# Kernel tuning notes

Measured on AMD Instinct MI355X. Metric: run time of the kernel, lower is better.

## Reference

```python
import jax, jax.numpy as jnp
import numpy as np

N_NODES = 65536
N_EDGES = 1048576
IN_FEATS = 128
H1 = 128
H2 = 256
N_CLASSES = 16


def setup_inputs() -> dict:
    key = jax.random.key(0)
    ks = jax.random.split(key, 12)
    s = 0.05
    x = jax.random.normal(ks[0], (N_NODES, IN_FEATS), dtype=jnp.float32)
    src = jax.random.randint(ks[1], (N_EDGES,), 0, N_NODES, dtype=jnp.int32)
    dst = jax.random.randint(ks[2], (N_EDGES,), 0, N_NODES, dtype=jnp.int32)
    # SAGEConv('pool') params: fc_pool (bias), fc_self (no bias), fc_neigh (no bias), output bias
    Wp = jax.random.normal(ks[3], (H1, IN_FEATS), dtype=jnp.float32) * s
    bp = jnp.zeros((H1,), dtype=jnp.float32)
    Ws = jax.random.normal(ks[4], (H1, IN_FEATS), dtype=jnp.float32) * s
    Wn = jax.random.normal(ks[5], (H1, H1), dtype=jnp.float32) * s
    bn = jnp.zeros((H1,), dtype=jnp.float32)
    # MLP head
    W1 = jax.random.normal(ks[6], (H2, H1), dtype=jnp.float32) * s
    b1 = jnp.zeros((H2,), dtype=jnp.float32)
    W2 = jax.random.normal(ks[7], (N_CLASSES, H2), dtype=jnp.float32) * s
    b2 = jnp.zeros((N_CLASSES,), dtype=jnp.float32)
    return {"x": x, "Wp": Wp, "bp": bp, "Ws": Ws, "Wn": Wn, "bn": bn,
            "W1": W1, "b1": b1, "W2": W2, "b2": b2, "src": src, "dst": dst}


def reference(x, Wp, bp, Ws, Wn, bn, W1, b1, W2, b2, src, dst):
    N = x.shape[0]
    # SAGEConv 'pool': per-edge MLP on gathered source features, segment-max over dst
    m = jax.nn.relu(x[src] @ Wp.T + bp)              # [E, H1]
    pooled = jax.ops.segment_max(m, dst, num_segments=N)  # [N, H1], -inf for isolated
    pooled = jnp.where(jnp.isneginf(pooled), 0.0, pooled)
    h = x @ Ws.T + pooled @ Wn.T + bn                # combine self + neigh
    h = jax.nn.leaky_relu(h)                         # slope 0.01 matches torch default
    h = jax.nn.leaky_relu(h @ W1.T + b1)
    # dropout is identity in eval mode
    h = jax.nn.sigmoid(h @ W2.T + b2)
    return h
```

## Files before the change

### kernel.cpp

```cpp
#include <hip/hip_runtime.h>
#include <cstdint>
#include <cstddef>

typedef __attribute__((ext_vector_type(8))) __bf16 bf16x8;
typedef __attribute__((ext_vector_type(4))) float f32x4;

union bf8pack { unsigned short u[8]; bf16x8 v; uint4 q; };

#define BCAP 768

static __device__ __forceinline__ unsigned short f2b(float f) {
    union { float f; unsigned int u; } v; v.f = f;
    unsigned int u = v.u;
    unsigned int r = (u + 0x7fffu + ((u >> 16) & 1u)) >> 16;
    return (unsigned short)r;
}

__global__ __launch_bounds__(256) void scatter_conv(
    const int* __restrict__ src, const int* __restrict__ dst,
    int* __restrict__ bcnt, unsigned int* __restrict__ pairs,
    const float* __restrict__ Wp, const float* __restrict__ Ws,
    const float* __restrict__ Wn, const float* __restrict__ W1,
    const float* __restrict__ W2,
    unsigned short* __restrict__ Wp_b, unsigned short* __restrict__ Wcat,
    unsigned short* __restrict__ W1_b, unsigned short* __restrict__ W2_b)
{
    const int tid = threadIdx.x;
    if ((int)blockIdx.x >= 256) {
        int i = ((int)blockIdx.x - 256) * 256 + tid;
        if (i < 16384) {
            Wp_b[i] = f2b(Wp[i]);
        } else if (i < 49152) {
            int j = i - 16384; int o = j >> 8, k = j & 255;
            Wcat[j] = f2b(k < 128 ? Ws[o * 128 + k] : Wn[o * 128 + (k - 128)]);
        } else if (i < 81920) {
            W1_b[i - 49152] = f2b(W1[i - 49152]);
        } else if (i < 86016) {
            W2_b[i - 81920] = f2b(W2[i - 81920]);
        }
        return;
    }
    __shared__ int h[2048];
    __shared__ int base_l[2048];
    __shared__ int cnt[2048];
    for (int i = tid; i < 2048; i += 256) { h[i] = 0; cnt[i] = 0; }
    __syncthreads();
    int base = blockIdx.x * 4096;
    int d_r[16], s_r[16];
#pragma unroll
    for (int i = 0; i < 16; i++) {
        int e = base + i * 256 + tid;
        d_r[i] = dst[e]; s_r[i] = src[e];
        atomicAdd(&h[((unsigned)d_r[i]) >> 5], 1);
    }
    __syncthreads();
    for (int i = tid; i < 2048; i += 256)
        base_l[i] = h[i] ? (i * BCAP + atomicAdd(&bcnt[i], h[i])) : 0;
    __syncthreads();
#pragma unroll
    for (int i = 0; i < 16; i++) {
        int b = ((unsigned)d_r[i]) >> 5;
        int pos = base_l[b] + atomicAdd(&cnt[b], 1);
        if (pos < (b + 1) * BCAP)
            pairs[pos] = ((unsigned)s_r[i] << 5) | ((unsigned)d_r[i] & 31u);
    }
}

__global__ __launch_bounds__(256) void k1_fused(
    const float* __restrict__ x, const unsigned short* __restrict__ Wp_b,
    const float* __restrict__ bias, unsigned short* __restrict__ bufX,
    unsigned short* __restrict__ y)
{
    const int bm = blockIdx.x;
    const int w  = threadIdx.x >> 6;
    const int wm = w & 1, wn = w >> 1;
    const int l  = threadIdx.x & 63;
    const int lr = l & 15, quad = l >> 4;
    const int m0 = bm * 128 + wm * 64;
    const int n0 = wn * 64;

    f32x4 acc[4][4];
#pragma unroll
    for (int i = 0; i < 4; i++)
#pragma unroll
        for (int j = 0; j < 4; j++) acc[i][j] = (f32x4){0.f, 0.f, 0.f, 0.f};

    const float* Ap = x + (size_t)(m0 + lr) * 128 + quad * 8;
    const unsigned short* Bp = Wp_b + (size_t)(n0 + lr) * 128 + quad * 8;

#pragma unroll
    for (int ks = 0; ks < 4; ks++) {
        bf16x8 af[4], bf[4];
#pragma unroll
        for (int i = 0; i < 4; i++) {
            const float* p = Ap + (size_t)i * 16 * 128 + ks * 32;
            float4 f0 = *(const float4*)p;
            float4 f1 = *(const float4*)(p + 4);
            bf8pack pk;
            pk.u[0] = f2b(f0.x); pk.u[1] = f2b(f0.y);
            pk.u[2] = f2b(f0.z); pk.u[3] = f2b(f0.w);
            pk.u[4] = f2b(f1.x); pk.u[5] = f2b(f1.y);
            pk.u[6] = f2b(f1.z); pk.u[7] = f2b(f1.w);
            af[i] = pk.v;
            if (wn == 0)
                *(uint4*)(bufX + (size_t)(m0 + lr + i * 16) * 256 + ks * 32 + quad * 8) = pk.q;
        }
#pragma unroll
        for (int i = 0; i < 4; i++)
            bf[i] = *(const bf16x8*)(Bp + (size_t)i * 16 * 128 + ks * 32);
#pragma unroll
        for (int mi = 0; mi < 4; mi++)
#pragma unroll
            for (int ni = 0; ni < 4; ni++)
                acc[mi][ni] = __builtin_amdgcn_mfma_f32_16x16x32_bf16(
                    af[mi], bf[ni], acc[mi][ni], 0, 0, 0);
    }

#pragma unroll
    for (int ni = 0; ni < 4; ni++) {
        const int col = n0 + ni * 16 + lr;
        const float bv = bias[col];
#pragma unroll
        for (int mi = 0; mi < 4; mi++) {
#pragma unroll
            for (int r = 0; r < 4; r++) {
                const int row = m0 + mi * 16 + quad * 4 + r;
                float v = acc[mi][ni][r] + bv;
                v = v > 0.f ? v : 0.f;
                y[(size_t)row * 128 + col] = f2b(v);
            }
        }
    }
}

__global__ __launch_bounds__(256) void bucket_pool3(
    const unsigned int* __restrict__ yu, const int* __restrict__ bcnt,
    const unsigned int* __restrict__ pairs, unsigned short* __restrict__ bufX)
{
    __shared__ unsigned short ldsSrc[1024];
    __shared__ int bin[32], offl[32], cnt2[32];
    const int b = blockIdx.x;
    const int tid = threadIdx.x;
    if (tid < 32) { bin[tid] = 0; cnt2[tid] = 0; }
    __syncthreads();
    const int beg = b * BCAP;
    int nb = bcnt[b]; nb = nb < 1024 ? nb : 1024;

    for (int i = tid; i < nb; i += 256)
        atomicAdd(&bin[pairs[beg + i] & 31u], 1);
    __syncthreads();
    if (tid == 0) {
        int run = 0;
        for (int i = 0; i < 32; i++) { offl[i] = run; run += bin[i]; }
    }
    __syncthreads();
    for (int i = tid; i < nb; i += 256) {
        unsigned int p = pairs[beg + i];
        int d = p & 31u;
        int slot = offl[d] + atomicAdd(&cnt2[d], 1);
        ldsSrc[slot] = (unsigned short)(p >> 5);
    }
    __syncthreads();

    const int w = tid >> 6, lane = tid & 63;
    for (int ni = 0; ni < 8; ni++) {
        const int n = w * 8 + ni;
        const int e0 = offl[n], cnt = bin[n];
        float ax = 0.f, ay = 0.f;
        for (int e = 0; e < cnt; e += 8) {
            int s[8]; unsigned int v[8];
#pragma unroll
            for (int j = 0; j < 8; j++) {
                int idx = e + j; idx = idx < cnt ? idx : cnt - 1;
                s[j] = ldsSrc[e0 + idx];
            }
#pragma unroll
            for (int j = 0; j < 8; j++) v[j] = yu[(size_t)s[j] * 64 + lane];
#pragma unroll
            for (int j = 0; j < 8; j++) {
                ax = fmaxf(ax, __uint_as_float(v[j] << 16));
                ay = fmaxf(ay, __uint_as_float(v[j] & 0xffff0000u));
            }
        }
        unsigned int packed = (__float_as_uint(ax) >> 16) | (__float_as_uint(ay) & 0xffff0000u);
        ((unsigned int*)bufX)[(size_t)(b * 32 + n) * 128 + 64 + lane] = packed;
    }
}

__global__ __launch_bounds__(256) void k4_gemm(
    const unsigned short* __restrict__ A,
    const unsigned short* __restrict__ W,
    const float* __restrict__ bias,
    unsigned short* __restrict__ C)
{
    const int bm = (int)blockIdx.x;
    const int w  = threadIdx.x >> 6;
    const int wm = w & 1, wn = w >> 1;
    const int l  = threadIdx.x & 63;
    const int lr = l & 15, quad = l >> 4;
    const int m0 = bm * 128 + wm * 64;
    const int n0 = wn * 64;

    f32x4 acc[4][4];
#pragma unroll
    for (int i = 0; i < 4; i++)
#pragma unroll
        for (int j = 0; j < 4; j++) acc[i][j] = (f32x4){0.f, 0.f, 0.f, 0.f};

    const unsigned short* Ap = A + (size_t)(m0 + lr) * 256 + quad * 8;
    const unsigned short* Bp = W + (size_t)(n0 + lr) * 256 + quad * 8;

    for (int ks = 0; ks < 8; ks++) {
        bf16x8 af[4], bf[4];
#pragma unroll
        for (int i = 0; i < 4; i++)
            af[i] = *(const bf16x8*)(Ap + (size_t)i * 16 * 256 + ks * 32);
#pragma unroll
        for (int i = 0; i < 4; i++)
            bf[i] = *(const bf16x8*)(Bp + (size_t)i * 16 * 256 + ks * 32);
#pragma unroll
        for (int mi = 0; mi < 4; mi++)
#pragma unroll
            for (int ni = 0; ni < 4; ni++)
                acc[mi][ni] = __builtin_amdgcn_mfma_f32_16x16x32_bf16(
                    af[mi], bf[ni], acc[mi][ni], 0, 0, 0);
    }

#pragma unroll
    for (int ni = 0; ni < 4; ni++) {
        const int col = n0 + ni * 16 + lr;
        const float bv = bias[col];
#pragma unroll
        for (int mi = 0; mi < 4; mi++) {
#pragma unroll
            for (int r = 0; r < 4; r++) {
                const int row = m0 + mi * 16 + quad * 4 + r;
                float v = acc[mi][ni][r] + bv;
                v = v > 0.f ? v : 0.01f * v;
                C[(size_t)row * 128 + col] = f2b(v);
            }
        }
    }
}

__global__ __launch_bounds__(256) void k5_head(
    const unsigned short* __restrict__ hbuf, const unsigned short* __restrict__ W1_b,
    const float* __restrict__ b1, const unsigned short* __restrict__ W2_b,
    const float* __restrict__ b2, float* __restrict__ out)
{
    __shared__ unsigned short H2[64 * 264];
    const int tid = threadIdx.x;
    const int w = tid >> 6, l = tid & 63;
    const int lr = l & 15, quad = l >> 4;
    const int wm = w & 1, wn = w >> 1;
    const int row0 = blockIdx.x * 64;

    f32x4 acc[2][8];
#pragma unroll
    for (int i = 0; i < 2; i++)
#pragma unroll
        for (int j = 0; j < 8; j++) acc[i][j] = (f32x4){0.f, 0.f, 0.f, 0.f};

    const unsigned short* Ag = hbuf + (size_t)(row0 + wm * 32 + lr) * 128 + quad * 8;
    const unsigned short* Bp = W1_b + (size_t)(wn * 128 + lr) * 128 + quad * 8;

#pragma unroll
    for (int ks = 0; ks < 4; ks++) {
        bf16x8 af[2], bfr[8];
#pragma unroll
        for (int i = 0; i < 2; i++)
            af[i] = *(const bf16x8*)(Ag + (size_t)i * 16 * 128 + ks * 32);
#pragma unroll
        for (int i = 0; i < 8; i++)
            bfr[i] = *(const bf16x8*)(Bp + (size_t)i * 16 * 128 + ks * 32);
#pragma unroll
        for (int mi = 0; mi < 2; mi++)
#pragma unroll
            for (int ni = 0; ni < 8; ni++)
                acc[mi][ni] = __builtin_amdgcn_mfma_f32_16x16x32_bf16(
                    af[mi], bfr[ni], acc[mi][ni], 0, 0, 0);
    }

#pragma unroll
    for (int ni = 0; ni < 8; ni++) {
        const int col = wn * 128 + ni * 16 + lr;
        const float bv = b1[col];
#pragma unroll
        for (int mi = 0; mi < 2; mi++) {
#pragma unroll
            for (int r = 0; r < 4; r++) {
                const int row = wm * 32 + mi * 16 + quad * 4 + r;
                float v = acc[mi][ni][r] + bv;
                v = v > 0.f ? v : 0.01f * v;
                H2[row * 264 + col] = f2b(v);
            }
        }
    }
    __syncthreads();

    const int m0 = w * 16;
    f32x4 a2 = (f32x4){0.f, 0.f, 0.f, 0.f};
#pragma unroll
    for (int ks = 0; ks < 8; ks++) {
        bf16x8 a = *(const bf16x8*)&H2[(m0 + lr) * 264 + ks * 32 + quad * 8];
        bf16x8 bb = *(const bf16x8*)(W2_b + (size_t)lr * 256 + ks * 32 + quad * 8);
        a2 = __builtin_amdgcn_mfma_f32_16x16x32_bf16(a, bb, a2, 0, 0, 0);
    }
    const float bv = b2[lr];
#pragma unroll
    for (int r = 0; r < 4; r++) {
        const int row = row0 + m0 + quad * 4 + r;
        float v = a2[r] + bv;
        out[(size_t)row * 16 + lr] = 1.f / (1.f + __expf(-v));
    }
}

extern "C" void kernel_launch(void* const* d_in, const int* in_sizes, int n_in,
                              void* d_out, int out_size, void* d_ws, size_t ws_size,
                              hipStream_t stream)
{
    const float* x  = (const float*)d_in[0];
    const float* Wp = (const float*)d_in[1];
    const float* bp = (const float*)d_in[2];
    const float* Ws = (const float*)d_in[3];
    const float* Wn = (const float*)d_in[4];
    const float* bn = (const float*)d_in[5];
    const float* W1 = (const float*)d_in[6];
    const float* b1 = (const float*)d_in[7];
    const float* W2 = (const float*)d_in[8];
    const float* b2 = (const float*)d_in[9];
    const int* src  = (const int*)d_in[10];
    const int* dst  = (const int*)d_in[11];
    float* out = (float*)d_out;

    const int N = in_sizes[0] / 128;

    unsigned short* bufX = (unsigned short*)d_ws;
    unsigned short* y    = (unsigned short*)((char*)d_ws + (size_t)32 * 1024 * 1024);
    unsigned short* hbuf = (unsigned short*)((char*)d_ws + (size_t)48 * 1024 * 1024);

    unsigned short* Wp_b = (unsigned short*)((char*)d_ws + (size_t)96 * 1024 * 1024);
    unsigned short* Wcat = Wp_b + 16384;
    unsigned short* W1_b = Wcat + 32768;
    unsigned short* W2_b = W1_b + 32768;
    int* bcnt = (int*)(W2_b + 4096);
    unsigned int* pairs = (unsigned int*)(bcnt + 2048);

    dim3 blk(256);

    hipMemsetAsync(bcnt, 0, 2048 * sizeof(int), stream);

    scatter_conv<<<592, blk, 0, stream>>>(src, dst, bcnt, pairs,
                                          Wp, Ws, Wn, W1, W2,
                                          Wp_b, Wcat, W1_b, W2_b);

    k1_fused<<<N / 128, blk, 0, stream>>>(x, Wp_b, bp, bufX, y);

    bucket_pool3<<<2048, blk, 0, stream>>>((const unsigned int*)y, bcnt, pairs, bufX);

    k4_gemm<<<N / 128, blk, 0, stream>>>(bufX, Wcat, bn, hbuf);

    k5_head<<<N / 64, blk, 0, stream>>>(hbuf, W1_b, b1, W2_b, b2, out);
}
```

Before: 218.3 us.

## Merge scatter, weight conversion and edge GEMM; fuse combine GEMM into MLP head

The edge-binning scatter, the weight conversion and the x·Wp GEMM now run as one launch. The GEMM converts Wp from fp32 inline, so it no longer depends on a separate conversion pass. The self/neighbour combine GEMM is folded into the head kernel: it reads x directly (converting to bf16) plus a compact pooled buffer, and keeps the hidden activation in LDS. This removes the bf16 copy of x and the hbuf round trip, cuts two launches, and uses vectorised int4 index loads. In exchange, the head kernel needs more LDS and recomputes the x conversion, and the edge GEMM does redundant fp32→bf16 conversion of Wp in every block.

```diff
diff --git a/kernel.cpp b/kernel.cpp
--- a/kernel.cpp
+++ b/kernel.cpp
@@ -16,43 +16,117 @@
     return (unsigned short)r;
 }
 
-__global__ __launch_bounds__(256) void scatter_conv(
+static __device__ __forceinline__ bf16x8 cvt8(const float* __restrict__ p) {
+    float4 f0 = *(const float4*)p;
+    float4 f1 = *(const float4*)(p + 4);
+    bf8pack pk;
+    pk.u[0] = f2b(f0.x); pk.u[1] = f2b(f0.y);
+    pk.u[2] = f2b(f0.z); pk.u[3] = f2b(f0.w);
+    pk.u[4] = f2b(f1.x); pk.u[5] = f2b(f1.y);
+    pk.u[6] = f2b(f1.z); pk.u[7] = f2b(f1.w);
+    return pk.v;
+}
+
+__global__ __launch_bounds__(256) void mega0(
     const int* __restrict__ src, const int* __restrict__ dst,
     int* __restrict__ bcnt, unsigned int* __restrict__ pairs,
-    const float* __restrict__ Wp, const float* __restrict__ Ws,
-    const float* __restrict__ Wn, const float* __restrict__ W1,
-    const float* __restrict__ W2,
-    unsigned short* __restrict__ Wp_b, unsigned short* __restrict__ Wcat,
-    unsigned short* __restrict__ W1_b, unsigned short* __restrict__ W2_b)
+    const float* __restrict__ x, const float* __restrict__ Wp,
+    const float* __restrict__ bp,
+    const float* __restrict__ Ws, const float* __restrict__ Wn,
+    const float* __restrict__ W1, const float* __restrict__ W2,
+    unsigned short* __restrict__ Wcat, unsigned short* __restrict__ W1_b,
+    unsigned short* __restrict__ W2_b, unsigned short* __restrict__ y)
 {
     const int tid = threadIdx.x;
-    if ((int)blockIdx.x >= 256) {
-        int i = ((int)blockIdx.x - 256) * 256 + tid;
-        if (i < 16384) {
-            Wp_b[i] = f2b(Wp[i]);
-        } else if (i < 49152) {
-            int j = i - 16384; int o = j >> 8, k = j & 255;
-            Wcat[j] = f2b(k < 128 ? Ws[o * 128 + k] : Wn[o * 128 + (k - 128)]);
-        } else if (i < 81920) {
-            W1_b[i - 49152] = f2b(W1[i - 49152]);
-        } else if (i < 86016) {
-            W2_b[i - 81920] = f2b(W2[i - 81920]);
+    const int bx = (int)blockIdx.x;
+
+    if (bx >= 768) {
+        int i = (bx - 768) * 256 + tid;
+        if (i < 32768) {
+            int o = i >> 8, k = i & 255;
+            Wcat[i] = f2b(k < 128 ? Ws[o * 128 + k] : Wn[o * 128 + (k - 128)]);
+        } else if (i < 65536) {
+            W1_b[i - 32768] = f2b(W1[i - 32768]);
+        } else {
+            W2_b[i - 65536] = f2b(W2[i - 65536]);
         }
         return;
     }
+
+    if (bx >= 256) {
+        const int bm = bx - 256;
+        const int w  = tid >> 6;
+        const int wm = w & 1, wn = w >> 1;
+        const int l  = tid & 63;
+        const int lr = l & 15, quad = l >> 4;
+        const int m0 = bm * 128 + wm * 64;
+        const int n0 = wn * 64;
+
+        f32x4 acc[4][4];
+#pragma unroll
+        for (int i = 0; i < 4; i++)
+#pragma unroll
+            for (int j = 0; j < 4; j++) acc[i][j] = (f32x4){0.f, 0.f, 0.f, 0.f};
+
+        const float* Apf = x  + (size_t)(m0 + lr) * 128 + quad * 8;
+        const float* Bpf = Wp + (size_t)(n0 + lr) * 128 + quad * 8;
+
+#pragma unroll
+        for (int ks = 0; ks < 4; ks++) {
+            bf16x8 af[4], bf[4];
+#pragma unroll
+            for (int i = 0; i < 4; i++)
+                af[i] = cvt8(Apf + (size_t)i * 16 * 128 + ks * 32);
+#pragma unroll
+            for (int i = 0; i < 4; i++)
+                bf[i] = cvt8(Bpf + (size_t)i * 16 * 128 + ks * 32);
+#pragma unroll
+            for (int mi = 0; mi < 4; mi++)
+#pragma unroll
+                for (int ni = 0; ni < 4; ni++)
+                    acc[mi][ni] = __builtin_amdgcn_mfma_f32_16x16x32_bf16(
+                        af[mi], bf[ni], acc[mi][ni], 0, 0, 0);
+        }
+
+#pragma unroll
+        for (int ni = 0; ni < 4; ni++) {
+            const int col = n0 + ni * 16 + lr;
+            const float bv = bp[col];
+#pragma unroll
+            for (int mi = 0; mi < 4; mi++) {
+#pragma unroll
+                for (int r = 0; r < 4; r++) {
+                    const int row = m0 + mi * 16 + quad * 4 + r;
+                    float v = acc[mi][ni][r] + bv;
+                    v = v > 0.f ? v : 0.f;
+                    y[(size_t)row * 128 + col] = f2b(v);
+                }
+            }
+        }
+        return;
+    }
+
     __shared__ int h[2048];
     __shared__ int base_l[2048];
     __shared__ int cnt[2048];
     for (int i = tid; i < 2048; i += 256) { h[i] = 0; cnt[i] = 0; }
     __syncthreads();
-    int base = blockIdx.x * 4096;
+    const int base = bx * 4096;
     int d_r[16], s_r[16];
-#pragma unroll
-    for (int i = 0; i < 16; i++) {
-        int e = base + i * 256 + tid;
-        d_r[i] = dst[e]; s_r[i] = src[e];
+    const int4* s4 = (const int4*)(src + base);
+    const int4* d4 = (const int4*)(dst + base);
+#pragma unroll
+    for (int i = 0; i < 4; i++) {
+        int4 dv = d4[tid + i * 256];
+        int4 sv = s4[tid + i * 256];
+        d_r[i * 4 + 0] = dv.x; d_r[i * 4 + 1] = dv.y;
+        d_r[i * 4 + 2] = dv.z; d_r[i * 4 + 3] = dv.w;
+        s_r[i * 4 + 0] = sv.x; s_r[i * 4 + 1] = sv.y;
+        s_r[i * 4 + 2] = sv.z; s_r[i * 4 + 3] = sv.w;
+    }
+#pragma unroll
+    for (int i = 0; i < 16; i++)
         atomicAdd(&h[((unsigned)d_r[i]) >> 5], 1);
-    }
     __syncthreads();
     for (int i = tid; i < 2048; i += 256)
         base_l[i] = h[i] ? (i * BCAP + atomicAdd(&bcnt[i], h[i])) : 0;
@@ -66,76 +140,9 @@
     }
 }
 
-__global__ __launch_bounds__(256) void k1_fused(
-    const float* __restrict__ x, const unsigned short* __restrict__ Wp_b,
-    const float* __restrict__ bias, unsigned short* __restrict__ bufX,
-    unsigned short* __restrict__ y)
-{
-    const int bm = blockIdx.x;
-    const int w  = threadIdx.x >> 6;
-    const int wm = w & 1, wn = w >> 1;
-    const int l  = threadIdx.x & 63;
-    const int lr = l & 15, quad = l >> 4;
-    const int m0 = bm * 128 + wm * 64;
-    const int n0 = wn * 64;
-
-    f32x4 acc[4][4];
-#pragma unroll
-    for (int i = 0; i < 4; i++)
-#pragma unroll
-        for (int j = 0; j < 4; j++) acc[i][j] = (f32x4){0.f, 0.f, 0.f, 0.f};
-
-    const float* Ap = x + (size_t)(m0 + lr) * 128 + quad * 8;
-    const unsigned short* Bp = Wp_b + (size_t)(n0 + lr) * 128 + quad * 8;
-
-#pragma unroll
-    for (int ks = 0; ks < 4; ks++) {
-        bf16x8 af[4], bf[4];
-#pragma unroll
-        for (int i = 0; i < 4; i++) {
-            const float* p = Ap + (size_t)i * 16 * 128 + ks * 32;
-            float4 f0 = *(const float4*)p;
-            float4 f1 = *(const float4*)(p + 4);
-            bf8pack pk;
-            pk.u[0] = f2b(f0.x); pk.u[1] = f2b(f0.y);
-            pk.u[2] = f2b(f0.z); pk.u[3] = f2b(f0.w);
-            pk.u[4] = f2b(f1.x); pk.u[5] = f2b(f1.y);
-            pk.u[6] = f2b(f1.z); pk.u[7] = f2b(f1.w);
-            af[i] = pk.v;
-            if (wn == 0)
-                *(uint4*)(bufX + (size_t)(m0 + lr + i * 16) * 256 + ks * 32 + quad * 8) = pk.q;
-        }
-#pragma unroll
-        for (int i = 0; i < 4; i++)
-            bf[i] = *(const bf16x8*)(Bp + (size_t)i * 16 * 128 + ks * 32);
-#pragma unroll
-        for (int mi = 0; mi < 4; mi++)
-#pragma unroll
-            for (int ni = 0; ni < 4; ni++)
-                acc[mi][ni] = __builtin_amdgcn_mfma_f32_16x16x32_bf16(
-                    af[mi], bf[ni], acc[mi][ni], 0, 0, 0);
-    }
-
-#pragma unroll
-    for (int ni = 0; ni < 4; ni++) {
-        const int col = n0 + ni * 16 + lr;
-        const float bv = bias[col];
-#pragma unroll
-        for (int mi = 0; mi < 4; mi++) {
-#pragma unroll
-            for (int r = 0; r < 4; r++) {
-                const int row = m0 + mi * 16 + quad * 4 + r;
-                float v = acc[mi][ni][r] + bv;
-                v = v > 0.f ? v : 0.f;
-                y[(size_t)row * 128 + col] = f2b(v);
-            }
-        }
-    }
-}
-
 __global__ __launch_bounds__(256) void bucket_pool3(
     const unsigned int* __restrict__ yu, const int* __restrict__ bcnt,
-    const unsigned int* __restrict__ pairs, unsigned short* __restrict__ bufX)
+    const unsigned int* __restrict__ pairs, unsigned short* __restrict__ pooled)
 {
     __shared__ unsigned short ldsSrc[1024];
     __shared__ int bin[32], offl[32], cnt2[32];
@@ -144,7 +151,7 @@
     if (tid < 32) { bin[tid] = 0; cnt2[tid] = 0; }
     __syncthreads();
     const int beg = b * BCAP;
-    int nb = bcnt[b]; nb = nb < 1024 ? nb : 1024;
+    int nb = bcnt[b]; nb = nb < BCAP ? nb : BCAP;
 
     for (int i = tid; i < nb; i += 256)
         atomicAdd(&bin[pairs[beg + i] & 31u], 1);
@@ -183,71 +190,18 @@
             }
         }
         unsigned int packed = (__float_as_uint(ax) >> 16) | (__float_as_uint(ay) & 0xffff0000u);
-        ((unsigned int*)bufX)[(size_t)(b * 32 + n) * 128 + 64 + lane] = packed;
-    }
-}
-
-__global__ __launch_bounds__(256) void k4_gemm(
-    const unsigned short* __restrict__ A,
-    const unsigned short* __restrict__ W,
-    const float* __restrict__ bias,
-    unsigned short* __restrict__ C)
+        ((unsigned int*)pooled)[(size_t)(b * 32 + n) * 64 + lane] = packed;
+    }
+}
+
+__global__ __launch_bounds__(256) void k45(
+    const float* __restrict__ x, const unsigned short* __restrict__ pooled,
+    const unsigned short* __restrict__ Wcat, const float* __restrict__ bn,
+    const unsigned short* __restrict__ W1_b, const float* __restrict__ b1,
+    const unsigned short* __restrict__ W2_b, const float* __restrict__ b2,
+    float* __restrict__ out)
 {
-    const int bm = (int)blockIdx.x;
-    const int w  = threadIdx.x >> 6;
-    const int wm = w & 1, wn = w >> 1;
-    const int l  = threadIdx.x & 63;
-    const int lr = l & 15, quad = l >> 4;
-    const int m0 = bm * 128 + wm * 64;
-    const int n0 = wn * 64;
-
-    f32x4 acc[4][4];
-#pragma unroll
-    for (int i = 0; i < 4; i++)
-#pragma unroll
-        for (int j = 0; j < 4; j++) acc[i][j] = (f32x4){0.f, 0.f, 0.f, 0.f};
-
-    const unsigned short* Ap = A + (size_t)(m0 + lr) * 256 + quad * 8;
-    const unsigned short* Bp = W + (size_t)(n0 + lr) * 256 + quad * 8;
-
-    for (int ks = 0; ks < 8; ks++) {
-        bf16x8 af[4], bf[4];
-#pragma unroll
-        for (int i = 0; i < 4; i++)
-            af[i] = *(const bf16x8*)(Ap + (size_t)i * 16 * 256 + ks * 32);
-#pragma unroll
-        for (int i = 0; i < 4; i++)
-            bf[i] = *(const bf16x8*)(Bp + (size_t)i * 16 * 256 + ks * 32);
-#pragma unroll
-        for (int mi = 0; mi < 4; mi++)
-#pragma unroll
-            for (int ni = 0; ni < 4; ni++)
-                acc[mi][ni] = __builtin_amdgcn_mfma_f32_16x16x32_bf16(
-                    af[mi], bf[ni], acc[mi][ni], 0, 0, 0);
-    }
-
-#pragma unroll
-    for (int ni = 0; ni < 4; ni++) {
-        const int col = n0 + ni * 16 + lr;
-        const float bv = bias[col];
-#pragma unroll
-        for (int mi = 0; mi < 4; mi++) {
-#pragma unroll
-            for (int r = 0; r < 4; r++) {
-                const int row = m0 + mi * 16 + quad * 4 + r;
-                float v = acc[mi][ni][r] + bv;
-                v = v > 0.f ? v : 0.01f * v;
-                C[(size_t)row * 128 + col] = f2b(v);
-            }
-        }
-    }
-}
-
-__global__ __launch_bounds__(256) void k5_head(
-    const unsigned short* __restrict__ hbuf, const unsigned short* __restrict__ W1_b,
-    const float* __restrict__ b1, const unsigned short* __restrict__ W2_b,
-    const float* __restrict__ b2, float* __restrict__ out)
-{
+    __shared__ unsigned short Hs[64 * 136];
     __shared__ unsigned short H2[64 * 264];
     const int tid = threadIdx.x;
     const int w = tid >> 6, l = tid & 63;
@@ -255,44 +209,97 @@
     const int wm = w & 1, wn = w >> 1;
     const int row0 = blockIdx.x * 64;
 
-    f32x4 acc[2][8];
-#pragma unroll
-    for (int i = 0; i < 2; i++)
-#pragma unroll
-        for (int j = 0; j < 8; j++) acc[i][j] = (f32x4){0.f, 0.f, 0.f, 0.f};
-
-    const unsigned short* Ag = hbuf + (size_t)(row0 + wm * 32 + lr) * 128 + quad * 8;
-    const unsigned short* Bp = W1_b + (size_t)(wn * 128 + lr) * 128 + quad * 8;
-
-#pragma unroll
-    for (int ks = 0; ks < 4; ks++) {
-        bf16x8 af[2], bfr[8];
+    {
+        f32x4 acc[2][4];
 #pragma unroll
         for (int i = 0; i < 2; i++)
-            af[i] = *(const bf16x8*)(Ag + (size_t)i * 16 * 128 + ks * 32);
-#pragma unroll
-        for (int i = 0; i < 8; i++)
-            bfr[i] = *(const bf16x8*)(Bp + (size_t)i * 16 * 128 + ks * 32);
-#pragma unroll
-        for (int mi = 0; mi < 2; mi++)
-#pragma unroll
-            for (int ni = 0; ni < 8; ni++)
-                acc[mi][ni] = __builtin_amdgcn_mfma_f32_16x16x32_bf16(
-                    af[mi], bfr[ni], acc[mi][ni], 0, 0, 0);
-    }
-
-#pragma unroll
-    for (int ni = 0; ni < 8; ni++) {
-        const int col = wn * 128 + ni * 16 + lr;
-        const float bv = b1[col];
-#pragma unroll
-        for (int mi = 0; mi < 2; mi++) {
-#pragma unroll
-            for (int r = 0; r < 4; r++) {
-                const int row = wm * 32 + mi * 16 + quad * 4 + r;
-                float v = acc[mi][ni][r] + bv;
-                v = v > 0.f ? v : 0.01f * v;
-                H2[row * 264 + col] = f2b(v);
+#pragma unroll
+            for (int j = 0; j < 4; j++) acc[i][j] = (f32x4){0.f, 0.f, 0.f, 0.f};
+
+        const float* Axp = x + (size_t)(row0 + wm * 32 + lr) * 128 + quad * 8;
+        const unsigned short* App = pooled + (size_t)(row0 + wm * 32 + lr) * 128 + quad * 8;
+        const unsigned short* Bp = Wcat + (size_t)(wn * 64 + lr) * 256 + quad * 8;
+
+#pragma unroll
+        for (int ks = 0; ks < 8; ks++) {
+            bf16x8 af[2], bf[4];
+            if (ks < 4) {
+#pragma unroll
+                for (int i = 0; i < 2; i++)
+                    af[i] = cvt8(Axp + (size_t)i * 16 * 128 + ks * 32);
+            } else {
+#pragma unroll
+                for (int i = 0; i < 2; i++)
+                    af[i] = *(const bf16x8*)(App + (size_t)i * 16 * 128 + (ks - 4) * 32);
+            }
+#pragma unroll
+            for (int i = 0; i < 4; i++)
+                bf[i] = *(const bf16x8*)(Bp + (size_t)i * 16 * 256 + ks * 32);
+#pragma unroll
+            for (int mi = 0; mi < 2; mi++)
+#pragma unroll
+                for (int ni = 0; ni < 4; ni++)
+                    acc[mi][ni] = __builtin_amdgcn_mfma_f32_16x16x32_bf16(
+                        af[mi], bf[ni], acc[mi][ni], 0, 0, 0);
+        }
+
+#pragma unroll
+        for (int ni = 0; ni < 4; ni++) {
+            const int col = wn * 64 + ni * 16 + lr;
+            const float bv = bn[col];
+#pragma unroll
+            for (int mi = 0; mi < 2; mi++) {
+#pragma unroll
+                for (int r = 0; r < 4; r++) {
+                    const int row = wm * 32 + mi * 16 + quad * 4 + r;
+                    float v = acc[mi][ni][r] + bv;
+                    v = v > 0.f ? v : 0.01f * v;
+                    Hs[row * 136 + col] = f2b(v);
+                }
+            }
+        }
+    }
+    __syncthreads();
+
+    {
+        f32x4 acc[2][8];
+#pragma unroll
+        for (int i = 0; i < 2; i++)
+#pragma unroll
+            for (int j = 0; j < 8; j++) acc[i][j] = (f32x4){0.f, 0.f, 0.f, 0.f};
+
+        const unsigned short* Bp = W1_b + (size_t)(wn * 128 + lr) * 128 + quad * 8;
+
+#pragma unroll
+        for (int ks = 0; ks < 4; ks++) {
+            bf16x8 af[2], bfr[8];
+#pragma unroll
+            for (int i = 0; i < 2; i++)
+                af[i] = *(const bf16x8*)&Hs[(wm * 32 + i * 16 + lr) * 136 + ks * 32 + quad * 8];
+#pragma unroll
+            for (int i = 0; i < 8; i++)
+                bfr[i] = *(const bf16x8*)(Bp + (size_t)i * 16 * 128 + ks * 32);
+#pragma unroll
+            for (int mi = 0; mi < 2; mi++)
+#pragma unroll
+                for (int ni = 0; ni < 8; ni++)
+                    acc[mi][ni] = __builtin_amdgcn_mfma_f32_16x16x32_bf16(
+                        af[mi], bfr[ni], acc[mi][ni], 0, 0, 0);
+        }
+
+#pragma unroll
+        for (int ni = 0; ni < 8; ni++) {
+            const int col = wn * 128 + ni * 16 + lr;
+            const float bv = b1[col];
+#pragma unroll
+            for (int mi = 0; mi < 2; mi++) {
+#pragma unroll
+                for (int r = 0; r < 4; r++) {
+                    const int row = wm * 32 + mi * 16 + quad * 4 + r;
+                    float v = acc[mi][ni][r] + bv;
+                    v = v > 0.f ? v : 0.01f * v;
+                    H2[row * 264 + col] = f2b(v);
+                }
             }
         }
     }
@@ -335,12 +342,9 @@
 
     const int N = in_sizes[0] / 128;
 
-    unsigned short* bufX = (unsigned short*)d_ws;
-    unsigned short* y    = (unsigned short*)((char*)d_ws + (size_t)32 * 1024 * 1024);
-    unsigned short* hbuf = (unsigned short*)((char*)d_ws + (size_t)48 * 1024 * 1024);
-
-    unsigned short* Wp_b = (unsigned short*)((char*)d_ws + (size_t)96 * 1024 * 1024);
-    unsigned short* Wcat = Wp_b + 16384;
+    unsigned short* y      = (unsigned short*)d_ws;
+    unsigned short* pooled = (unsigned short*)((char*)d_ws + (size_t)16 * 1024 * 1024);
+    unsigned short* Wcat   = (unsigned short*)((char*)d_ws + (size_t)32 * 1024 * 1024);
     unsigned short* W1_b = Wcat + 32768;
     unsigned short* W2_b = W1_b + 32768;
     int* bcnt = (int*)(W2_b + 4096);
@@ -350,15 +354,11 @@
 
     hipMemsetAsync(bcnt, 0, 2048 * sizeof(int), stream);
 
-    scatter_conv<<<592, blk, 0, stream>>>(src, dst, bcnt, pairs,
-                                          Wp, Ws, Wn, W1, W2,
-                                          Wp_b, Wcat, W1_b, W2_b);
-
-    k1_fused<<<N / 128, blk, 0, stream>>>(x, Wp_b, bp, bufX, y);
-
-    bucket_pool3<<<2048, blk, 0, stream>>>((const unsigned int*)y, bcnt, pairs, bufX);
-
-    k4_gemm<<<N / 128, blk, 0, stream>>>(bufX, Wcat, bn, hbuf);
-
-    k5_head<<<N / 64, blk, 0, stream>>>(hbuf, W1_b, b1, W2_b, b2, out);
-}
+    mega0<<<1040, blk, 0, stream>>>(src, dst, bcnt, pairs,
+                                    x, Wp, bp, Ws, Wn, W1, W2,
+                                    Wcat, W1_b, W2_b, y);
+
+    bucket_pool3<<<2048, blk, 0, stream>>>((const unsigned int*)y, bcnt, pairs, pooled);
+
+    k45<<<N / 64, blk, 0, stream>>>(x, pooled, Wcat, bn, W1_b, b1, W2_b, b2, out);
+}
```

After: 212.8 us. -2.5%, faster.
